# Performance work log

Measured on AMD Instinct MI355X. Metric: run time of the kernel, lower is better.

The kernel has to match this reference:

```python
import jax, jax.numpy as jnp
import numpy as np

# fixed-point config (matches init_kwargs)
DIM, H = 768, 12
DHEAD = DIM // H
DATA_W, DATA_F = 32, 16        # input activation quantizer
WQ = WK = WV = WP = (16, 8)    # weight quantizers (width, frac)
BQ = BK = BV = BP = (16, 8)    # bias quantizers
DQ = DK = DV = DS = DZ = (16, 8)  # activation quantizers after each stage
OUT_W, OUT_F = 32, 8


def qfix(x, width, frac):
    """Fixed-point integer quantizer: round to 2^-frac grid, clamp to signed width."""
    scale = jnp.float32(2.0 ** frac)
    lo = -(2.0 ** (width - 1))
    hi = 2.0 ** (width - 1) - 1
    return jnp.clip(jnp.round(x * scale), lo, hi) / scale


def setup_inputs() -> dict:
    key = jax.random.key(0)
    ks = jax.random.split(key, 5)
    return {
        "q_in": jax.random.normal(ks[0], (2, 2048, DIM), dtype=jnp.float32),
        "wqkv": jax.random.normal(ks[1], (3 * DIM, DIM), dtype=jnp.float32) * 0.05,
        "bqkv": jax.random.normal(ks[2], (3 * DIM,), dtype=jnp.float32) * 0.05,
        "wp": jax.random.normal(ks[3], (DIM, DIM), dtype=jnp.float32) * 0.05,
        "bp": jax.random.normal(ks[4], (DIM,), dtype=jnp.float32) * 0.05,
    }


def reference(q_in, wqkv, bqkv, wp, bp):
    B, N, _ = q_in.shape
    # per-head weight split: wqkv -> (H, 3*DHEAD, DIM), rows [0:d]=q, [d:2d]=k, [2d:3d]=v
    w = wqkv.reshape(H, 3 * DHEAD, DIM)
    b = bqkv.reshape(H, 3 * DHEAD)
    wq_, wk_, wv_ = w[:, :DHEAD], w[:, DHEAD:2 * DHEAD], w[:, 2 * DHEAD:]
    bq_, bk_, bv_ = b[:, :DHEAD], b[:, DHEAD:2 * DHEAD], b[:, 2 * DHEAD:]

    x = qfix(q_in, DATA_W, DATA_F)  # QuantizedLinear input quantization

    def qlin(wt, bt, wcfg, bcfg, ocfg):
        # y[b,h,n,e] = x[b,n,d] @ qw[h,e,d]^T + qb[h,e], then output quantize
        y = jnp.einsum('bnd,hed->bhne', x, qfix(wt, *wcfg)) + qfix(bt, *bcfg)[None, :, None, :]
        return qfix(y, *ocfg)

    q = qlin(wq_, bq_, WQ, BQ, DQ)  # (B,H,N,DHEAD)
    k = qlin(wk_, bk_, WK, BK, DK)
    v = qlin(wv_, bv_, WV, BV, DV)

    s = qfix(jnp.einsum('bhne,bhme->bhnm', q, k), *DS)   # (B,H,N,N) quantized scores
    z = qfix(jnp.einsum('bhnm,bhme->bhne', s, v), *DZ)   # (B,H,N,DHEAD)

    # concat heads along feature dim (torch.cat dim=2)
    zc = z.transpose(0, 2, 1, 3).reshape(B, N, DIM)

    # quantized projection: input quantized with data_z cfg (idempotent here)
    out = jnp.einsum('bnd,ed->bne', qfix(zc, *DZ), qfix(wp, *WP)) + qfix(bp, *BP)
    return qfix(out, OUT_W, OUT_F)
```

## Files before the change

### kernel.cpp

```cpp
#include <hip/hip_runtime.h>


#define NTOK 4096
#define DIM  768
#define NH   12
#define DH   64
#define SEQ  2048
#define QKVD 2304
#define NBH  24
#define LSTR 72

typedef _Float16 half8 __attribute__((ext_vector_type(8)));
typedef _Float16 half4 __attribute__((ext_vector_type(4)));
typedef __fp16   fp16x2 __attribute__((ext_vector_type(2)));
typedef float floatx4 __attribute__((ext_vector_type(4)));

__global__ __launch_bounds__(256) void prep(
    const float* __restrict__ X,
    const float* __restrict__ wqkv, const float* __restrict__ bqkv,
    const float* __restrict__ wp,   const float* __restrict__ bp,
    _Float16* __restrict__ Xh, _Float16* __restrict__ Xl,
    _Float16* __restrict__ W16, _Float16* __restrict__ Wp16,
    float* __restrict__ bq24, float* __restrict__ bp16)
{
    int i = blockIdx.x * 256 + threadIdx.x;
    int i4 = i * 4;
    if (i4 < NTOK * DIM) {
        float4 x = *(const float4*)(X + i4);
        float xi[4] = {x.x, x.y, x.z, x.w};
        half4 oh, ol;
#pragma unroll
        for (int j = 0; j < 4; ++j) {
            float v = rintf(xi[j] * 65536.0f);
            float h = rintf(v * (1.0f / 2048.0f));
            ((_Float16*)&oh)[j] = (_Float16)h;
            ((_Float16*)&ol)[j] = (_Float16)(v - 2048.0f * h);
        }
        *(half4*)(Xh + i4) = oh;
        *(half4*)(Xl + i4) = ol;
    }
    if (i4 < QKVD * DIM) {
        float4 w = *(const float4*)(wqkv + i4);
        half4 o = {(_Float16)rintf(w.x * 256.0f), (_Float16)rintf(w.y * 256.0f),
                   (_Float16)rintf(w.z * 256.0f), (_Float16)rintf(w.w * 256.0f)};
        *(half4*)(W16 + i4) = o;
    }
    if (i4 < DIM * DIM) {
        float4 w = *(const float4*)(wp + i4);
        half4 o = {(_Float16)rintf(w.x * 256.0f), (_Float16)rintf(w.y * 256.0f),
                   (_Float16)rintf(w.z * 256.0f), (_Float16)rintf(w.w * 256.0f)};
        *(half4*)(Wp16 + i4) = o;
    }
    if (i < QKVD) bq24[i] = rintf(bqkv[i] * 256.0f) * 65536.0f;
    if (i < DIM)  bp16[i] = rintf(bp[i] * 256.0f) * 256.0f;
}

__global__ __launch_bounds__(256) void qkv_mfma(
    const _Float16* __restrict__ Xh, const _Float16* __restrict__ Xl,
    const _Float16* __restrict__ W16, const float* __restrict__ bq24,
    _Float16* __restrict__ Q16, _Float16* __restrict__ K16,
    _Float16* __restrict__ Vt16)
{
    __shared__ __align__(16) _Float16 Ah[64 * LSTR];
    __shared__ __align__(16) _Float16 Al[64 * LSTR];
    __shared__ __align__(16) _Float16 Bs[128 * LSTR];
    const int t = threadIdx.x;
    const int wave = t >> 6, lane = t & 63;
    const int lrow = lane & 15, quad = lane >> 4;
    const int m0 = blockIdx.y * 64;
    const int col0 = blockIdx.x * 128;

    floatx4 acch[4][2], accl[4][2];
#pragma unroll
    for (int fm = 0; fm < 4; ++fm)
#pragma unroll
        for (int fn = 0; fn < 2; ++fn) {
            acch[fm][fn] = (floatx4){0.f, 0.f, 0.f, 0.f};
            accl[fm][fn] = (floatx4){0.f, 0.f, 0.f, 0.f};
        }

    for (int k0 = 0; k0 < DIM; k0 += 64) {
        __syncthreads();
#pragma unroll
        for (int i = 0; i < 2; ++i) {
            int id = t + 256 * i;
            int r = id >> 3, c8 = id & 7;
            *(half8*)(&Ah[r * LSTR + c8 * 8]) =
                *(const half8*)(Xh + (size_t)(m0 + r) * DIM + k0 + c8 * 8);
            *(half8*)(&Al[r * LSTR + c8 * 8]) =
                *(const half8*)(Xl + (size_t)(m0 + r) * DIM + k0 + c8 * 8);
        }
#pragma unroll
        for (int i = 0; i < 4; ++i) {
            int id = t + 256 * i;
            int r = id >> 3, c8 = id & 7;
            *(half8*)(&Bs[r * LSTR + c8 * 8]) =
                *(const half8*)(W16 + (size_t)(col0 + r) * DIM + k0 + c8 * 8);
        }
        __syncthreads();
#pragma unroll
        for (int kk = 0; kk < 64; kk += 32) {
            half8 bf[2];
#pragma unroll
            for (int fn = 0; fn < 2; ++fn)
                bf[fn] = *(const half8*)(&Bs[(wave * 32 + fn * 16 + lrow) * LSTR + kk + quad * 8]);
#pragma unroll
            for (int fm = 0; fm < 4; ++fm) {
                half8 ah = *(const half8*)(&Ah[(fm * 16 + lrow) * LSTR + kk + quad * 8]);
                half8 al = *(const half8*)(&Al[(fm * 16 + lrow) * LSTR + kk + quad * 8]);
#pragma unroll
                for (int fn = 0; fn < 2; ++fn) {
                    acch[fm][fn] = __builtin_amdgcn_mfma_f32_16x16x32_f16(ah, bf[fn], acch[fm][fn], 0, 0, 0);
                    accl[fm][fn] = __builtin_amdgcn_mfma_f32_16x16x32_f16(al, bf[fn], accl[fm][fn], 0, 0, 0);
                }
            }
        }
    }

    const int b_ = m0 >> 11;
    const int n0base = m0 & 2047;
#pragma unroll
    for (int fn = 0; fn < 2; ++fn) {
        const int c = col0 + wave * 32 + fn * 16 + lrow;
        const int h = c / 192;
        const int jj = c % 192;
        const int kind = jj >> 6;
        const int e = jj & 63;
        const int bh = b_ * NH + h;
        const float bb = bq24[c];
#pragma unroll
        for (int fm = 0; fm < 4; ++fm) {
            float qv[4];
#pragma unroll
            for (int rg = 0; rg < 4; ++rg) {
                float y = fmaf(2048.0f, acch[fm][fn][rg], accl[fm][fn][rg]) + bb;
                float q = rintf(y * (1.0f / 65536.0f));
                qv[rg] = fminf(fmaxf(q, -32768.0f), 32767.0f);
            }
            const int n0 = n0base + fm * 16 + quad * 4;
            if (kind == 2) {
                half4 o = {(_Float16)qv[0], (_Float16)qv[1], (_Float16)qv[2], (_Float16)qv[3]};
                *(half4*)(Vt16 + ((size_t)bh * DH + e) * SEQ + n0) = o;
            } else {
                _Float16* dst = (kind == 0) ? Q16 : K16;
#pragma unroll
                for (int rg = 0; rg < 4; ++rg)
                    dst[((size_t)bh * SEQ + n0 + rg) * DH + e] = (_Float16)qv[rg];
            }
        }
    }
}

__global__ __launch_bounds__(256) void attention_mfma(
    const _Float16* __restrict__ Q16, const _Float16* __restrict__ K16,
    const _Float16* __restrict__ Vt16,
    _Float16* __restrict__ Zh16, _Float16* __restrict__ Zl16)
{
    __shared__ __align__(16) _Float16 Qs[64 * LSTR];
    __shared__ __align__(16) _Float16 Ks[64 * LSTR];
    __shared__ __align__(16) _Float16 Vs[64 * LSTR];
    __shared__ __align__(16) _Float16 Shs[64 * LSTR];
    __shared__ __align__(16) _Float16 Sls[64 * LSTR];
    const int t = threadIdx.x;
    const int bh = blockIdx.x;
    const int qt = blockIdx.y;
    const int wave = t >> 6, lane = t & 63;
    const int lrow = lane & 15, quad = lane >> 4;
    const _Float16* Qg = Q16 + ((size_t)bh * SEQ + qt * 64) * DH;
    const _Float16* Kg = K16 + (size_t)bh * SEQ * DH;
    const _Float16* Vg = Vt16 + (size_t)bh * DH * SEQ;

    {
        int r = t >> 3, k8 = t & 7;
        *(half8*)(&Qs[r * LSTR + k8 * 8]) = *(const half8*)(Qg + r * DH + k8 * 8);
        int t2 = t + 256; int r2 = t2 >> 3, k82 = t2 & 7;
        *(half8*)(&Qs[r2 * LSTR + k82 * 8]) = *(const half8*)(Qg + r2 * DH + k82 * 8);
    }

    floatx4 zh[4], zl[4];
#pragma unroll
    for (int nt = 0; nt < 4; ++nt) {
        zh[nt] = (floatx4){0.f, 0.f, 0.f, 0.f};
        zl[nt] = (floatx4){0.f, 0.f, 0.f, 0.f};
    }
    const int qrow = (wave * 16 + lrow) * LSTR;

    for (int m0 = 0; m0 < SEQ; m0 += 64) {
        __syncthreads();
        {
            int r = t >> 3, k8 = t & 7;
            *(half8*)(&Ks[r * LSTR + k8 * 8]) =
                *(const half8*)(Kg + (size_t)(m0 + r) * DH + k8 * 8);
            *(half8*)(&Vs[r * LSTR + k8 * 8]) =
                *(const half8*)(Vg + (size_t)r * SEQ + m0 + k8 * 8);
            int t2 = t + 256; int r2 = t2 >> 3, k82 = t2 & 7;
            *(half8*)(&Ks[r2 * LSTR + k82 * 8]) =
                *(const half8*)(Kg + (size_t)(m0 + r2) * DH + k82 * 8);
            *(half8*)(&Vs[r2 * LSTR + k82 * 8]) =
                *(const half8*)(Vg + (size_t)r2 * SEQ + m0 + k82 * 8);
        }
        __syncthreads();

        floatx4 sc[4];
#pragma unroll
        for (int nt = 0; nt < 4; ++nt) sc[nt] = (floatx4){0.f, 0.f, 0.f, 0.f};
#pragma unroll
        for (int kk = 0; kk < 64; kk += 32) {
            half8 qf = *(const half8*)(&Qs[qrow + kk + quad * 8]);
#pragma unroll
            for (int nt = 0; nt < 4; ++nt) {
                half8 kf = *(const half8*)(&Ks[(nt * 16 + lrow) * LSTR + kk + quad * 8]);
                sc[nt] = __builtin_amdgcn_mfma_f32_16x16x32_f16(kf, qf, sc[nt], 0, 0, 0);
            }
        }
#pragma unroll
        for (int nt = 0; nt < 4; ++nt) {
            float shv[4], slv[4];
#pragma unroll
            for (int rg = 0; rg < 4; ++rg) {
                float v = rintf(sc[nt][rg] * 0.00390625f);
                v = fminf(fmaxf(v, -32768.0f), 32767.0f);
                float hh = rintf(v * (1.0f / 2048.0f));
                shv[rg] = hh;
                slv[rg] = fmaf(-2048.0f, hh, v);
            }
            union { fp16x2 p[2]; half4 v; } uh, ul;
            uh.p[0] = __builtin_amdgcn_cvt_pkrtz(shv[0], shv[1]);
            uh.p[1] = __builtin_amdgcn_cvt_pkrtz(shv[2], shv[3]);
            ul.p[0] = __builtin_amdgcn_cvt_pkrtz(slv[0], slv[1]);
            ul.p[1] = __builtin_amdgcn_cvt_pkrtz(slv[2], slv[3]);
            *(half4*)(&Shs[qrow + nt * 16 + quad * 4]) = uh.v;
            *(half4*)(&Sls[qrow + nt * 16 + quad * 4]) = ul.v;
        }
        __threadfence_block();

#pragma unroll
        for (int kk = 0; kk < 64; kk += 32) {
            half8 ah = *(const half8*)(&Shs[qrow + kk + quad * 8]);
            half8 al = *(const half8*)(&Sls[qrow + kk + quad * 8]);
#pragma unroll
            for (int nt = 0; nt < 4; ++nt) {
                half8 vf = *(const half8*)(&Vs[(nt * 16 + lrow) * LSTR + kk + quad * 8]);
                zh[nt] = __builtin_amdgcn_mfma_f32_16x16x32_f16(ah, vf, zh[nt], 0, 0, 0);
                zl[nt] = __builtin_amdgcn_mfma_f32_16x16x32_f16(al, vf, zl[nt], 0, 0, 0);
            }
        }
    }

    const int b_ = bh / NH, h = bh % NH;
#pragma unroll
    for (int nt = 0; nt < 4; ++nt)
#pragma unroll
        for (int rg = 0; rg < 4; ++rg) {
            float zint = fmaf(2048.0f, zh[nt][rg], zl[nt][rg]);
            float zq = rintf(zint * 0.00390625f);
            zq = fminf(fmaxf(zq, -32768.0f), 32767.0f);
            float zdh = rintf(zq * (1.0f / 2048.0f));
            float zdl = zq - 2048.0f * zdh;
            int n = qt * 64 + wave * 16 + quad * 4 + rg;
            int e = nt * 16 + lrow;
            size_t off = ((size_t)b_ * SEQ + n) * DIM + h * DH + e;
            Zh16[off] = (_Float16)zdh;
            Zl16[off] = (_Float16)zdl;
        }
}

__global__ __launch_bounds__(256) void out_mfma(
    const _Float16* __restrict__ Zh, const _Float16* __restrict__ Zl,
    const _Float16* __restrict__ Wp16, const float* __restrict__ bp16,
    float* __restrict__ O)
{
    __shared__ __align__(16) _Float16 Ah[64 * LSTR];
    __shared__ __align__(16) _Float16 Al[64 * LSTR];
    __shared__ __align__(16) _Float16 Bs[128 * LSTR];
    const int t = threadIdx.x;
    const int wave = t >> 6, lane = t & 63;
    const int lrow = lane & 15, quad = lane >> 4;
    const int m0 = blockIdx.y * 64;
    const int col0 = blockIdx.x * 128;

    floatx4 acch[4][2], accl[4][2];
#pragma unroll
    for (int fm = 0; fm < 4; ++fm)
#pragma unroll
        for (int fn = 0; fn < 2; ++fn) {
            acch[fm][fn] = (floatx4){0.f, 0.f, 0.f, 0.f};
            accl[fm][fn] = (floatx4){0.f, 0.f, 0.f, 0.f};
        }

    for (int k0 = 0; k0 < DIM; k0 += 64) {
        __syncthreads();
#pragma unroll
        for (int i = 0; i < 2; ++i) {
            int id = t + 256 * i;
            int r = id >> 3, c8 = id & 7;
            *(half8*)(&Ah[r * LSTR + c8 * 8]) =
                *(const half8*)(Zh + (size_t)(m0 + r) * DIM + k0 + c8 * 8);
            *(half8*)(&Al[r * LSTR + c8 * 8]) =
                *(const half8*)(Zl + (size_t)(m0 + r) * DIM + k0 + c8 * 8);
        }
#pragma unroll
        for (int i = 0; i < 4; ++i) {
            int id = t + 256 * i;
            int r = id >> 3, c8 = id & 7;
            *(half8*)(&Bs[r * LSTR + c8 * 8]) =
                *(const half8*)(Wp16 + (size_t)(col0 + r) * DIM + k0 + c8 * 8);
        }
        __syncthreads();
#pragma unroll
        for (int kk = 0; kk < 64; kk += 32) {
            half8 bf[2];
#pragma unroll
            for (int fn = 0; fn < 2; ++fn)
                bf[fn] = *(const half8*)(&Bs[(wave * 32 + fn * 16 + lrow) * LSTR + kk + quad * 8]);
#pragma unroll
            for (int fm = 0; fm < 4; ++fm) {
                half8 ah = *(const half8*)(&Ah[(fm * 16 + lrow) * LSTR + kk + quad * 8]);
                half8 al = *(const half8*)(&Al[(fm * 16 + lrow) * LSTR + kk + quad * 8]);
#pragma unroll
                for (int fn = 0; fn < 2; ++fn) {
                    acch[fm][fn] = __builtin_amdgcn_mfma_f32_16x16x32_f16(ah, bf[fn], acch[fm][fn], 0, 0, 0);
                    accl[fm][fn] = __builtin_amdgcn_mfma_f32_16x16x32_f16(al, bf[fn], accl[fm][fn], 0, 0, 0);
                }
            }
        }
    }

#pragma unroll
    for (int fn = 0; fn < 2; ++fn) {
        const int c = col0 + wave * 32 + fn * 16 + lrow;
        const float bb = bp16[c];
#pragma unroll
        for (int fm = 0; fm < 4; ++fm)
#pragma unroll
            for (int rg = 0; rg < 4; ++rg) {
                float y = fmaf(2048.0f, acch[fm][fn][rg], accl[fm][fn][rg]) + bb;
                float o = rintf(y * 0.00390625f) * 0.00390625f;
                int r = m0 + fm * 16 + quad * 4 + rg;
                O[(size_t)r * DIM + c] = o;
            }
    }
}

extern "C" void kernel_launch(void* const* d_in, const int* in_sizes, int n_in,
                              void* d_out, int out_size, void* d_ws, size_t ws_size,
                              hipStream_t stream) {
    const float* q_in = (const float*)d_in[0];
    const float* wqkv = (const float*)d_in[1];
    const float* bqkv = (const float*)d_in[2];
    const float* wp   = (const float*)d_in[3];
    const float* bp   = (const float*)d_in[4];

    char* w = (char*)d_ws;
    _Float16* W16  = (_Float16*)w;  w += (size_t)QKVD * DIM * 2;
    _Float16* Wp16 = (_Float16*)w;  w += (size_t)DIM * DIM * 2;
    float* bq24    = (float*)w;     w += QKVD * 4;
    float* bp16    = (float*)w;     w += DIM * 4;
    _Float16* Xh   = (_Float16*)w;  w += (size_t)NTOK * DIM * 2;
    _Float16* Xl   = (_Float16*)w;  w += (size_t)NTOK * DIM * 2;
    _Float16* Q16  = (_Float16*)w;  w += (size_t)NBH * SEQ * DH * 2;
    _Float16* K16  = (_Float16*)w;  w += (size_t)NBH * SEQ * DH * 2;
    _Float16* Vt16 = (_Float16*)w;  w += (size_t)NBH * SEQ * DH * 2;
    _Float16* Zh16 = (_Float16*)w;  w += (size_t)NTOK * DIM * 2;
    _Float16* Zl16 = (_Float16*)w;  w += (size_t)NTOK * DIM * 2;
    (void)ws_size; (void)in_sizes; (void)n_in; (void)out_size;

    prep<<<dim3(NTOK * DIM / 4 / 256), 256, 0, stream>>>(
        q_in, wqkv, bqkv, wp, bp, Xh, Xl, W16, Wp16, bq24, bp16);
    qkv_mfma<<<dim3(QKVD / 128, NTOK / 64), 256, 0, stream>>>(
        Xh, Xl, W16, bq24, Q16, K16, Vt16);
    attention_mfma<<<dim3(NBH, SEQ / 64), 256, 0, stream>>>(Q16, K16, Vt16, Zh16, Zl16);
    out_mfma<<<dim3(DIM / 128, NTOK / 64), 256, 0, stream>>>(
        Zh16, Zl16, Wp16, bp16, (float*)d_out);
}
```

Baseline: 208.5 us.

## Keep Q fragments in registers and share one score LDS buffer to cut LDS

The attention kernel no longer stages Q in shared memory: each lane loads its two Q fragments directly into registers once. The separate high and low score buffers become a single buffer that is written and consumed twice in sequence, and V fragments are preloaded into registers for both passes. LDS per block drops from five tiles to three, and launch bounds request three blocks per CU, aiming for higher occupancy. In exchange, register pressure rises and there is an extra intra-wave LDS write/read round with a block-level fence.

```diff
diff --git a/kernel.cpp b/kernel.cpp
--- a/kernel.cpp
+++ b/kernel.cpp
@@ -151,16 +151,14 @@
     }
 }
 
-__global__ __launch_bounds__(256) void attention_mfma(
+__global__ __launch_bounds__(256, 3) void attention_mfma(
     const _Float16* __restrict__ Q16, const _Float16* __restrict__ K16,
     const _Float16* __restrict__ Vt16,
     _Float16* __restrict__ Zh16, _Float16* __restrict__ Zl16)
 {
-    __shared__ __align__(16) _Float16 Qs[64 * LSTR];
     __shared__ __align__(16) _Float16 Ks[64 * LSTR];
     __shared__ __align__(16) _Float16 Vs[64 * LSTR];
-    __shared__ __align__(16) _Float16 Shs[64 * LSTR];
-    __shared__ __align__(16) _Float16 Sls[64 * LSTR];
+    __shared__ __align__(16) _Float16 Ss[64 * LSTR];
     const int t = threadIdx.x;
     const int bh = blockIdx.x;
     const int qt = blockIdx.y;
@@ -170,12 +168,8 @@
     const _Float16* Kg = K16 + (size_t)bh * SEQ * DH;
     const _Float16* Vg = Vt16 + (size_t)bh * DH * SEQ;
 
-    {
-        int r = t >> 3, k8 = t & 7;
-        *(half8*)(&Qs[r * LSTR + k8 * 8]) = *(const half8*)(Qg + r * DH + k8 * 8);
-        int t2 = t + 256; int r2 = t2 >> 3, k82 = t2 & 7;
-        *(half8*)(&Qs[r2 * LSTR + k82 * 8]) = *(const half8*)(Qg + r2 * DH + k82 * 8);
-    }
+    const half8 qf0 = *(const half8*)(Qg + (wave * 16 + lrow) * DH + 0  + quad * 8);
+    const half8 qf1 = *(const half8*)(Qg + (wave * 16 + lrow) * DH + 32 + quad * 8);
 
     floatx4 zh[4], zl[4];
 #pragma unroll
@@ -205,14 +199,14 @@
 #pragma unroll
         for (int nt = 0; nt < 4; ++nt) sc[nt] = (floatx4){0.f, 0.f, 0.f, 0.f};
 #pragma unroll
-        for (int kk = 0; kk < 64; kk += 32) {
-            half8 qf = *(const half8*)(&Qs[qrow + kk + quad * 8]);
-#pragma unroll
-            for (int nt = 0; nt < 4; ++nt) {
-                half8 kf = *(const half8*)(&Ks[(nt * 16 + lrow) * LSTR + kk + quad * 8]);
-                sc[nt] = __builtin_amdgcn_mfma_f32_16x16x32_f16(kf, qf, sc[nt], 0, 0, 0);
-            }
-        }
+        for (int nt = 0; nt < 4; ++nt) {
+            half8 kf0 = *(const half8*)(&Ks[(nt * 16 + lrow) * LSTR + 0  + quad * 8]);
+            half8 kf1 = *(const half8*)(&Ks[(nt * 16 + lrow) * LSTR + 32 + quad * 8]);
+            sc[nt] = __builtin_amdgcn_mfma_f32_16x16x32_f16(kf0, qf0, sc[nt], 0, 0, 0);
+            sc[nt] = __builtin_amdgcn_mfma_f32_16x16x32_f16(kf1, qf1, sc[nt], 0, 0, 0);
+        }
+
+        half4 hv[4], lv[4];
 #pragma unroll
         for (int nt = 0; nt < 4; ++nt) {
             float shv[4], slv[4];
@@ -229,20 +223,41 @@
             uh.p[1] = __builtin_amdgcn_cvt_pkrtz(shv[2], shv[3]);
             ul.p[0] = __builtin_amdgcn_cvt_pkrtz(slv[0], slv[1]);
             ul.p[1] = __builtin_amdgcn_cvt_pkrtz(slv[2], slv[3]);
-            *(half4*)(&Shs[qrow + nt * 16 + quad * 4]) = uh.v;
-            *(half4*)(&Sls[qrow + nt * 16 + quad * 4]) = ul.v;
-        }
+            hv[nt] = uh.v;
+            lv[nt] = ul.v;
+        }
+
+        half8 vf0[4], vf1[4];
+#pragma unroll
+        for (int nt = 0; nt < 4; ++nt) {
+            vf0[nt] = *(const half8*)(&Vs[(nt * 16 + lrow) * LSTR + 0  + quad * 8]);
+            vf1[nt] = *(const half8*)(&Vs[(nt * 16 + lrow) * LSTR + 32 + quad * 8]);
+        }
+
+#pragma unroll
+        for (int nt = 0; nt < 4; ++nt)
+            *(half4*)(&Ss[qrow + nt * 16 + quad * 4]) = hv[nt];
         __threadfence_block();
-
-#pragma unroll
-        for (int kk = 0; kk < 64; kk += 32) {
-            half8 ah = *(const half8*)(&Shs[qrow + kk + quad * 8]);
-            half8 al = *(const half8*)(&Sls[qrow + kk + quad * 8]);
+        {
+            half8 a0 = *(const half8*)(&Ss[qrow + 0  + quad * 8]);
+            half8 a1 = *(const half8*)(&Ss[qrow + 32 + quad * 8]);
 #pragma unroll
             for (int nt = 0; nt < 4; ++nt) {
-                half8 vf = *(const half8*)(&Vs[(nt * 16 + lrow) * LSTR + kk + quad * 8]);
-                zh[nt] = __builtin_amdgcn_mfma_f32_16x16x32_f16(ah, vf, zh[nt], 0, 0, 0);
-                zl[nt] = __builtin_amdgcn_mfma_f32_16x16x32_f16(al, vf, zl[nt], 0, 0, 0);
+                zh[nt] = __builtin_amdgcn_mfma_f32_16x16x32_f16(a0, vf0[nt], zh[nt], 0, 0, 0);
+                zh[nt] = __builtin_amdgcn_mfma_f32_16x16x32_f16(a1, vf1[nt], zh[nt], 0, 0, 0);
+            }
+        }
+#pragma unroll
+        for (int nt = 0; nt < 4; ++nt)
+            *(half4*)(&Ss[qrow + nt * 16 + quad * 4]) = lv[nt];
+        __threadfence_block();
+        {
+            half8 a0 = *(const half8*)(&Ss[qrow + 0  + quad * 8]);
+            half8 a1 = *(const half8*)(&Ss[qrow + 32 + quad * 8]);
+#pragma unroll
+            for (int nt = 0; nt < 4; ++nt) {
+                zl[nt] = __builtin_amdgcn_mfma_f32_16x16x32_f16(a0, vf0[nt], zl[nt], 0, 0, 0);
+                zl[nt] = __builtin_amdgcn_mfma_f32_16x16x32_f16(a1, vf1[nt], zl[nt], 0, 0, 0);
             }
         }
     }
```

Result: no change. 206.4 us (-1.0%).

## Rework attention kernel to 32x32 MFMA tiles with register-resident scores

Applied to the files above, without the earlier changes.

Rewrites the attention kernel to use 32x32x16 MFMA tiles. Each wave computes a 32x32 score block, and Q is kept in registers instead of shared memory. Quantized score hi/lo halves are exchanged between lanes with shuffles instead of round-tripping through LDS, which removes the Q/S shared buffers and the fence. Waves split the key dimension, so partial Z accumulators are reduced across waves through a shared scratch at the end. The output is written as vectorized half4 stores, and an occupancy hint of 3 blocks per CU is added, with added register pressure and a final reduction as the cost.

```diff
diff --git a/kernel.cpp b/kernel.cpp
--- a/kernel.cpp
+++ b/kernel.cpp
@@ -14,6 +14,7 @@
 typedef _Float16 half4 __attribute__((ext_vector_type(4)));
 typedef __fp16   fp16x2 __attribute__((ext_vector_type(2)));
 typedef float floatx4 __attribute__((ext_vector_type(4)));
+typedef float floatx16 __attribute__((ext_vector_type(16)));
 
 __global__ __launch_bounds__(256) void prep(
     const float* __restrict__ X,
@@ -151,39 +152,39 @@
     }
 }
 
-__global__ __launch_bounds__(256) void attention_mfma(
+__global__ __launch_bounds__(256, 3) void attention_mfma(
     const _Float16* __restrict__ Q16, const _Float16* __restrict__ K16,
     const _Float16* __restrict__ Vt16,
     _Float16* __restrict__ Zh16, _Float16* __restrict__ Zl16)
 {
-    __shared__ __align__(16) _Float16 Qs[64 * LSTR];
-    __shared__ __align__(16) _Float16 Ks[64 * LSTR];
-    __shared__ __align__(16) _Float16 Vs[64 * LSTR];
-    __shared__ __align__(16) _Float16 Shs[64 * LSTR];
-    __shared__ __align__(16) _Float16 Sls[64 * LSTR];
+    __shared__ __align__(16) char smem[64 * LSTR * 2 * 2];
+    _Float16* Ks = (_Float16*)smem;
+    _Float16* Vs = Ks + 64 * LSTR;
+    float* scr = (float*)smem;
+
     const int t = threadIdx.x;
     const int bh = blockIdx.x;
     const int qt = blockIdx.y;
-    const int wave = t >> 6, lane = t & 63;
-    const int lrow = lane & 15, quad = lane >> 4;
+    const int w = t >> 6, lane = t & 63;
+    const int l31 = lane & 31, hi = lane >> 5;
+    const int wj = w & 1;
+    const int wi = w >> 1;
     const _Float16* Qg = Q16 + ((size_t)bh * SEQ + qt * 64) * DH;
     const _Float16* Kg = K16 + (size_t)bh * SEQ * DH;
     const _Float16* Vg = Vt16 + (size_t)bh * DH * SEQ;
 
-    {
-        int r = t >> 3, k8 = t & 7;
-        *(half8*)(&Qs[r * LSTR + k8 * 8]) = *(const half8*)(Qg + r * DH + k8 * 8);
-        int t2 = t + 256; int r2 = t2 >> 3, k82 = t2 & 7;
-        *(half8*)(&Qs[r2 * LSTR + k82 * 8]) = *(const half8*)(Qg + r2 * DH + k82 * 8);
-    }
-
-    floatx4 zh[4], zl[4];
-#pragma unroll
-    for (int nt = 0; nt < 4; ++nt) {
-        zh[nt] = (floatx4){0.f, 0.f, 0.f, 0.f};
-        zl[nt] = (floatx4){0.f, 0.f, 0.f, 0.f};
-    }
-    const int qrow = (wave * 16 + lrow) * LSTR;
+    half8 qf[4];
+#pragma unroll
+    for (int i = 0; i < 4; ++i)
+        qf[i] = *(const half8*)(Qg + (32 * wj + l31) * DH + 16 * i + 8 * hi);
+
+    floatx16 acc[2][2];
+#pragma unroll
+    for (int d = 0; d < 2; ++d)
+#pragma unroll
+        for (int et = 0; et < 2; ++et)
+#pragma unroll
+            for (int r = 0; r < 16; ++r) acc[d][et][r] = 0.f;
 
     for (int m0 = 0; m0 < SEQ; m0 += 64) {
         __syncthreads();
@@ -201,68 +202,102 @@
         }
         __syncthreads();
 
-        floatx4 sc[4];
-#pragma unroll
-        for (int nt = 0; nt < 4; ++nt) sc[nt] = (floatx4){0.f, 0.f, 0.f, 0.f};
-#pragma unroll
-        for (int kk = 0; kk < 64; kk += 32) {
-            half8 qf = *(const half8*)(&Qs[qrow + kk + quad * 8]);
-#pragma unroll
-            for (int nt = 0; nt < 4; ++nt) {
-                half8 kf = *(const half8*)(&Ks[(nt * 16 + lrow) * LSTR + kk + quad * 8]);
-                sc[nt] = __builtin_amdgcn_mfma_f32_16x16x32_f16(kf, qf, sc[nt], 0, 0, 0);
-            }
-        }
-#pragma unroll
-        for (int nt = 0; nt < 4; ++nt) {
-            float shv[4], slv[4];
-#pragma unroll
-            for (int rg = 0; rg < 4; ++rg) {
-                float v = rintf(sc[nt][rg] * 0.00390625f);
-                v = fminf(fmaxf(v, -32768.0f), 32767.0f);
-                float hh = rintf(v * (1.0f / 2048.0f));
-                shv[rg] = hh;
-                slv[rg] = fmaf(-2048.0f, hh, v);
-            }
-            union { fp16x2 p[2]; half4 v; } uh, ul;
-            uh.p[0] = __builtin_amdgcn_cvt_pkrtz(shv[0], shv[1]);
-            uh.p[1] = __builtin_amdgcn_cvt_pkrtz(shv[2], shv[3]);
-            ul.p[0] = __builtin_amdgcn_cvt_pkrtz(slv[0], slv[1]);
-            ul.p[1] = __builtin_amdgcn_cvt_pkrtz(slv[2], slv[3]);
-            *(half4*)(&Shs[qrow + nt * 16 + quad * 4]) = uh.v;
-            *(half4*)(&Sls[qrow + nt * 16 + quad * 4]) = ul.v;
-        }
-        __threadfence_block();
-
-#pragma unroll
-        for (int kk = 0; kk < 64; kk += 32) {
-            half8 ah = *(const half8*)(&Shs[qrow + kk + quad * 8]);
-            half8 al = *(const half8*)(&Sls[qrow + kk + quad * 8]);
-#pragma unroll
-            for (int nt = 0; nt < 4; ++nt) {
-                half8 vf = *(const half8*)(&Vs[(nt * 16 + lrow) * LSTR + kk + quad * 8]);
-                zh[nt] = __builtin_amdgcn_mfma_f32_16x16x32_f16(ah, vf, zh[nt], 0, 0, 0);
-                zl[nt] = __builtin_amdgcn_mfma_f32_16x16x32_f16(al, vf, zl[nt], 0, 0, 0);
-            }
+        floatx16 sc;
+#pragma unroll
+        for (int r = 0; r < 16; ++r) sc[r] = 0.f;
+#pragma unroll
+        for (int i = 0; i < 4; ++i) {
+            half8 kf = *(const half8*)(&Ks[(32 * wi + l31) * LSTR + 16 * i + 8 * hi]);
+            sc = __builtin_amdgcn_mfma_f32_32x32x16_f16(kf, qf[i], sc, 0, 0, 0);
+        }
+
+        float hh[16], ll[16];
+#pragma unroll
+        for (int r = 0; r < 16; ++r) {
+            float v = rintf(sc[r] * 0.00390625f);
+            v = fminf(fmaxf(v, -32768.0f), 32767.0f);
+            float h = rintf(v * (1.0f / 2048.0f));
+            hh[r] = h;
+            ll[r] = fmaf(-2048.0f, h, v);
+        }
+        int dwh[4][2], dwl[4][2], swh[4][2], swl[4][2];
+        union { fp16x2 h; int i; } cv;
+#pragma unroll
+        for (int g = 0; g < 4; ++g) {
+            cv.h = __builtin_amdgcn_cvt_pkrtz(hh[4 * g + 0], hh[4 * g + 1]); dwh[g][0] = cv.i;
+            cv.h = __builtin_amdgcn_cvt_pkrtz(hh[4 * g + 2], hh[4 * g + 3]); dwh[g][1] = cv.i;
+            cv.h = __builtin_amdgcn_cvt_pkrtz(ll[4 * g + 0], ll[4 * g + 1]); dwl[g][0] = cv.i;
+            cv.h = __builtin_amdgcn_cvt_pkrtz(ll[4 * g + 2], ll[4 * g + 3]); dwl[g][1] = cv.i;
+        }
+#pragma unroll
+        for (int g = 0; g < 4; ++g) {
+            swh[g][0] = __shfl_xor(dwh[g][0], 32);
+            swh[g][1] = __shfl_xor(dwh[g][1], 32);
+            swl[g][0] = __shfl_xor(dwl[g][0], 32);
+            swl[g][1] = __shfl_xor(dwl[g][1], 32);
+        }
+
+        half8 vf[2][2];
+#pragma unroll
+        for (int et = 0; et < 2; ++et)
+#pragma unroll
+            for (int c = 0; c < 2; ++c)
+                vf[et][c] = *(const half8*)(&Vs[(32 * et + l31) * LSTR + 32 * wi + 16 * c + 8 * hi]);
+#pragma unroll
+        for (int c = 0; c < 2; ++c) {
+            union { int b[4]; half8 v; } ubh, ubl;
+            ubh.b[0] = hi ? swh[2 * c + 1][0] : dwh[2 * c][0];
+            ubh.b[1] = hi ? swh[2 * c + 1][1] : dwh[2 * c][1];
+            ubh.b[2] = hi ? dwh[2 * c + 1][0] : swh[2 * c][0];
+            ubh.b[3] = hi ? dwh[2 * c + 1][1] : swh[2 * c][1];
+            ubl.b[0] = hi ? swl[2 * c + 1][0] : dwl[2 * c][0];
+            ubl.b[1] = hi ? swl[2 * c + 1][1] : dwl[2 * c][1];
+            ubl.b[2] = hi ? dwl[2 * c + 1][0] : swl[2 * c][0];
+            ubl.b[3] = hi ? dwl[2 * c + 1][1] : swl[2 * c][1];
+#pragma unroll
+            for (int et = 0; et < 2; ++et) {
+                acc[0][et] = __builtin_amdgcn_mfma_f32_32x32x16_f16(vf[et][c], ubh.v, acc[0][et], 0, 0, 0);
+                acc[1][et] = __builtin_amdgcn_mfma_f32_32x32x16_f16(vf[et][c], ubl.v, acc[1][et], 0, 0, 0);
+            }
+        }
+    }
+
+#pragma unroll
+    for (int d = 0; d < 2; ++d) {
+        __syncthreads();
+#pragma unroll
+        for (int r = 0; r < 16; ++r) {
+            int er = (r & 3) + 8 * (r >> 2) + 4 * hi;
+            scr[((wj * 2 + (1 - wi)) * 32 + er) * 33 + l31] = acc[d][1 - wi][r];
+        }
+        __syncthreads();
+#pragma unroll
+        for (int r = 0; r < 16; ++r) {
+            int er = (r & 3) + 8 * (r >> 2) + 4 * hi;
+            acc[d][wi][r] += scr[((wj * 2 + wi) * 32 + er) * 33 + l31];
         }
     }
 
     const int b_ = bh / NH, h = bh % NH;
-#pragma unroll
-    for (int nt = 0; nt < 4; ++nt)
-#pragma unroll
-        for (int rg = 0; rg < 4; ++rg) {
-            float zint = fmaf(2048.0f, zh[nt][rg], zl[nt][rg]);
+    const int n = qt * 64 + 32 * wj + l31;
+    const size_t rowoff = ((size_t)b_ * SEQ + n) * DIM + h * DH;
+#pragma unroll
+    for (int g = 0; g < 4; ++g) {
+        int e0 = 32 * wi + 8 * g + 4 * hi;
+        half4 ph, pl;
+#pragma unroll
+        for (int j = 0; j < 4; ++j) {
+            int r = 4 * g + j;
+            float zint = fmaf(2048.0f, acc[0][wi][r], acc[1][wi][r]);
             float zq = rintf(zint * 0.00390625f);
             zq = fminf(fmaxf(zq, -32768.0f), 32767.0f);
             float zdh = rintf(zq * (1.0f / 2048.0f));
-            float zdl = zq - 2048.0f * zdh;
-            int n = qt * 64 + wave * 16 + quad * 4 + rg;
-            int e = nt * 16 + lrow;
-            size_t off = ((size_t)b_ * SEQ + n) * DIM + h * DH + e;
-            Zh16[off] = (_Float16)zdh;
-            Zl16[off] = (_Float16)zdl;
-        }
+            ((_Float16*)&ph)[j] = (_Float16)zdh;
+            ((_Float16*)&pl)[j] = (_Float16)(zq - 2048.0f * zdh);
+        }
+        *(half4*)(Zh16 + rowoff + e0) = ph;
+        *(half4*)(Zl16 + rowoff + e0) = pl;
+    }
 }
 
 __global__ __launch_bounds__(256) void out_mfma(
```

Measured after the change: 522.8 us. +150.7%, slower.
